# Kernel tuning notes

Hardware: AMD Instinct MI355X
Metric: run time of the kernel (lower is better)

Reference implementation:

```python
import jax, jax.numpy as jnp
import numpy as np

B, T, C, H = 2, 2048, 1024, 16
HD = C // H            # 64
LAYER_IDX, N_LAYER = 5, 12
BASE = 16
# window_mode='power_2.0': progress=(5+1)/12=0.5; window=max(16, int(16+0.5**2*(2048-16)))=524
WINDOW = max(BASE, int(BASE + ((LAYER_IDX + 1) / N_LAYER) ** 2.0 * (T - BASE)))
WINDOW = min(WINDOW, T)


def setup_inputs() -> dict:
    key = jax.random.key(0)
    ks = jax.random.split(key, 6)
    x = jax.random.normal(ks[0], (B, T, C), dtype=jnp.float32)
    Wq = jax.random.normal(ks[1], (C, C), dtype=jnp.float32) * 0.02
    Wk = jax.random.normal(ks[2], (C, C), dtype=jnp.float32) * 0.02
    Wv = jax.random.normal(ks[3], (C, C), dtype=jnp.float32) * 0.02
    Wo = jax.random.normal(ks[4], (C, C), dtype=jnp.float32) * 0.02
    # RoPE tables: angles theta_i = t / 10000^(i/(HD/2)), shape (T,1,HD//2) to broadcast over (B,T,H,HD//2)
    half = HD // 2
    inv_freq = 1.0 / (10000.0 ** (jnp.arange(half, dtype=jnp.float32) / half))
    ang = jnp.arange(T, dtype=jnp.float32)[:, None] * inv_freq[None, :]  # (T, half)
    rope_cos = jnp.cos(ang)[:, None, :]  # (T,1,half)
    rope_sin = jnp.sin(ang)[:, None, :]
    return {"x": x, "Wq": Wq, "Wk": Wk, "Wv": Wv, "Wo": Wo,
            "rope_cos": rope_cos, "rope_sin": rope_sin}


def _apply_rotary(x, cos, sin):
    d = x.shape[-1] // 2
    x1, x2 = x[..., :d], x[..., d:]
    return jnp.concatenate([x1 * cos + x2 * sin, -x2 * sin + x1 * cos], axis=-1)


def reference(x, Wq, Wk, Wv, Wo, rope_cos, rope_sin):
    Bv, Tv, Cv = x.shape
    q = (x @ Wq).reshape(Bv, Tv, H, HD)
    k = (x @ Wk).reshape(Bv, Tv, H, HD)
    v = (x @ Wv).reshape(Bv, Tv, H, HD)
    q = _apply_rotary(q, rope_cos, rope_sin)
    k = _apply_rotary(k, rope_cos, rope_sin)
    # sliding-window causal mask: cols<=rows and cols>=rows-WINDOW+1
    rows = jnp.arange(Tv)[:, None]
    cols = jnp.arange(Tv)[None, :]
    allowed = (cols <= rows) & (cols >= rows - WINDOW + 1)  # (T,T)
    scale = 1.0 / np.sqrt(HD)
    scores = jnp.einsum('bthd,bshd->bhts', q, k) * scale  # (B,H,T,T)
    scores = jnp.where(allowed[None, None], scores, -jnp.inf)
    attn = jax.nn.softmax(scores, axis=-1)
    y = jnp.einsum('bhts,bshd->bthd', attn, v).reshape(Bv, Tv, Cv)
    return y @ Wo
```

## Files before the change

kernel.cpp:

```cpp
#include <hip/hip_runtime.h>
#include <math.h>

typedef unsigned short u16;
typedef unsigned int u32;
typedef __bf16 bf16x8 __attribute__((ext_vector_type(8)));
typedef float f32x4 __attribute__((ext_vector_type(4)));
typedef unsigned short ushort4v __attribute__((ext_vector_type(4)));

#define T_SEQ 2048
#define WIN_M1 523
#define QSCALE 0.180336879f
#define MASKV -1e30f
#define MINIT -3000.0f

__device__ __forceinline__ u16 f2b(float f) {
  union { float f; unsigned int u; } v; v.f = f;
  unsigned int u = v.u;
  u += 0x7FFFu + ((u >> 16) & 1u);
  return (u16)(u >> 16);
}

__device__ __forceinline__ u32 cvtpk(float lo, float hi) {
  u32 r;
  asm("v_cvt_pk_bf16_f32 %0, %1, %2" : "=v"(r) : "v"(lo), "v"(hi));
  return r;
}

__device__ __forceinline__ void load_lds16(const u16* g, u16* l) {
  __builtin_amdgcn_global_load_lds(
      (const __attribute__((address_space(1))) void*)g,
      (__attribute__((address_space(3))) void*)l, 16, 0, 0);
}

__global__ void convert_x_k(const float* __restrict__ x, u16* __restrict__ xb) {
  int i = blockIdx.x * blockDim.x + threadIdx.x;
  float4 v = ((const float4*)x)[i];
  u16* d = xb + i * 4;
  d[0] = f2b(v.x); d[1] = f2b(v.y); d[2] = f2b(v.z); d[3] = f2b(v.w);
}

__global__ void transpose_w4_k(const float* __restrict__ W0, const float* __restrict__ W1,
                               const float* __restrict__ W2, const float* __restrict__ W3,
                               u16* __restrict__ WcatT, u16* __restrict__ WoT) {
  __shared__ float tile[32][33];
  const int z = blockIdx.z;
  const float* W = (z == 0) ? W0 : (z == 1) ? W1 : (z == 2) ? W2 : W3;
  u16* Wt = (z < 3) ? (WcatT + (size_t)z * 1024 * 1024) : WoT;
  int tx = threadIdx.x & 31, ty = threadIdx.x >> 5;
  int n0 = blockIdx.x * 32, k0 = blockIdx.y * 32;
#pragma unroll
  for (int i = 0; i < 4; ++i)
    tile[ty + i * 8][tx] = W[(size_t)(k0 + ty + i * 8) * 1024 + n0 + tx];
  __syncthreads();
#pragma unroll
  for (int i = 0; i < 4; ++i)
    Wt[(size_t)(n0 + ty + i * 8) * 1024 + k0 + tx] = f2b(tile[tx][ty + i * 8]);
}

template <int MODE>
__global__ __launch_bounds__(256, 4) void gemm_k(
    const u16* __restrict__ A, const u16* __restrict__ Bt,
    float* __restrict__ outf,
    u16* __restrict__ Qo, u16* __restrict__ Ko, u16* __restrict__ Vto,
    const float* __restrict__ rc, const float* __restrict__ rs) {
  __shared__ alignas(16) u16 As[2][128 * 32];
  __shared__ alignas(16) u16 Bs[2][128 * 32];
  const int tid = threadIdx.x, lane = tid & 63, w = tid >> 6;
  const int l15 = lane & 15, q4 = lane >> 4;
  const int row0 = blockIdx.y * 128, col0 = blockIdx.x * 128;
  const int wm = w >> 1, wn = w & 1;
  constexpr int NT = 32;

  f32x4 acc[4][4];
#pragma unroll
  for (int i = 0; i < 4; ++i)
#pragma unroll
    for (int j = 0; j < 4; ++j) acc[i][j] = (f32x4){0.f, 0.f, 0.f, 0.f};

  const int off0 = (w * 2) * 1024 + lane * 16;
  const int r0 = off0 >> 6, c0 = (off0 & 63) >> 1;
  const int off1 = off0 + 1024;
  const int r1 = off1 >> 6, c1 = (off1 & 63) >> 1;
  const u16* gA0 = A + (size_t)(row0 + r0) * 1024 + c0;
  const u16* gA1 = A + (size_t)(row0 + r1) * 1024 + c1;
  const u16* gB0 = Bt + (size_t)(col0 + r0) * 1024 + c0;
  const u16* gB1 = Bt + (size_t)(col0 + r1) * 1024 + c1;
  const int soff = (w * 2) * 512;

  auto stage = [&](int buf, int t) {
    const int k0 = t * 32;
    load_lds16(gA0 + k0, &As[buf][soff]);
    load_lds16(gA1 + k0, &As[buf][soff + 512]);
    load_lds16(gB0 + k0, &Bs[buf][soff]);
    load_lds16(gB1 + k0, &Bs[buf][soff + 512]);
  };
  auto compute = [&](int buf) {
    bf16x8 af[4], bfr[4];
#pragma unroll
    for (int im = 0; im < 4; ++im)
      af[im] = *(const bf16x8*)&As[buf][(wm * 64 + im * 16 + l15) * 32 + q4 * 8];
#pragma unroll
    for (int jn = 0; jn < 4; ++jn)
      bfr[jn] = *(const bf16x8*)&Bs[buf][(wn * 64 + jn * 16 + l15) * 32 + q4 * 8];
#pragma unroll
    for (int im = 0; im < 4; ++im)
#pragma unroll
      for (int jn = 0; jn < 4; ++jn)
        acc[im][jn] = __builtin_amdgcn_mfma_f32_16x16x32_bf16(af[im], bfr[jn], acc[im][jn], 0, 0, 0);
  };

  stage(0, 0);
  for (int t = 0; t + 1 < NT; ++t) {
    stage((t + 1) & 1, t + 1);
    asm volatile("s_waitcnt vmcnt(4)" ::: "memory");
    __builtin_amdgcn_s_barrier();
    compute(t & 1);
    __builtin_amdgcn_s_barrier();
  }
  asm volatile("s_waitcnt vmcnt(0)" ::: "memory");
  __builtin_amdgcn_s_barrier();
  compute((NT - 1) & 1);

  if constexpr (MODE == 0) {
#pragma unroll
    for (int im = 0; im < 4; ++im) {
      const int rowb = row0 + wm * 64 + im * 16 + q4 * 4;
      const int b = rowb >> 11, t0 = rowb & 2047;
#pragma unroll
      for (int jn = 0; jn < 2; ++jn) {
        const int n = col0 + wn * 64 + jn * 16 + l15;
        const int sel = n >> 10, nn = n & 1023;
        const int h = nn >> 6, hd = nn & 63;
        if (sel < 2) {
          const float qs = (sel == 0) ? QSCALE : 1.0f;
          u16* dst = (sel == 0 ? Qo : Ko) + ((size_t)(b * 16 + h) * 2048) * 64;
#pragma unroll
          for (int r = 0; r < 4; ++r) {
            const int tt = t0 + r;
            const float c = rc[tt * 32 + hd], s = rs[tt * 32 + hd];
            const float x1 = acc[im][jn][r], x2 = acc[im][jn + 2][r];
            dst[(size_t)tt * 64 + hd] = f2b((x1 * c + x2 * s) * qs);
            dst[(size_t)tt * 64 + hd + 32] = f2b((x1 * c - x2 * s) * qs);
          }
        } else {
          ushort4v p1, p2;
#pragma unroll
          for (int r = 0; r < 4; ++r) {
            p1[r] = f2b(acc[im][jn][r]);
            p2[r] = f2b(acc[im][jn + 2][r]);
          }
          u16* dst = Vto + (size_t)(b * 16 + h) * 64 * 2048 + t0;
          *(ushort4v*)(dst + (size_t)hd * 2048) = p1;
          *(ushort4v*)(dst + (size_t)(hd + 32) * 2048) = p2;
        }
      }
    }
  } else {
#pragma unroll
    for (int im = 0; im < 4; ++im) {
      const int rowb = row0 + wm * 64 + im * 16 + q4 * 4;
#pragma unroll
      for (int jn = 0; jn < 4; ++jn) {
        const int n = col0 + wn * 64 + jn * 16 + l15;
#pragma unroll
        for (int r = 0; r < 4; ++r)
          outf[(size_t)(rowb + r) * 1024 + n] = acc[im][jn][r];
      }
    }
  }
}

__global__ __launch_bounds__(256) void attn_k(
    const u16* __restrict__ Q, const u16* __restrict__ Kk,
    const u16* __restrict__ Vt, u16* __restrict__ Y) {
  const int lane = threadIdx.x & 63, w = threadIdx.x >> 6;
  const int l15 = lane & 15, q4 = lane >> 4;
  const int qt = blockIdx.x & 15, bh = blockIdx.x >> 4;
  const int q0 = qt * 128 + w * 32;
  const u16* Qb = Q + (size_t)bh * 2048 * 64;
  const u16* Kb = Kk + (size_t)bh * 2048 * 64;
  const u16* Vb = Vt + (size_t)bh * 64 * 2048;

  bf16x8 bq[2][2];
#pragma unroll
  for (int qs = 0; qs < 2; ++qs)
#pragma unroll
    for (int kb = 0; kb < 2; ++kb)
      bq[qs][kb] = *(const bf16x8*)(Qb + (size_t)(q0 + qs * 16 + l15) * 64 + kb * 32 + q4 * 8);

  f32x4 o[2][4];
#pragma unroll
  for (int qs = 0; qs < 2; ++qs)
#pragma unroll
    for (int jo = 0; jo < 4; ++jo) o[qs][jo] = (f32x4){0.f, 0.f, 0.f, 0.f};
  float m[2] = {MINIT, MINIT}, lsum[2] = {0.f, 0.f};

  int s0 = q0 - WIN_M1; if (s0 < 0) s0 = 0; s0 &= ~31;
  const int srcA = l15 + ((q4 & 1) << 5);
  const int srcB = srcA + 16;
  const bool lowq4 = (q4 < 2);

  bf16x8 kc[2][2], kn[2][2];
  bf16x8 vc[4], vn[4];
#pragma unroll
  for (int ks = 0; ks < 2; ++ks)
#pragma unroll
    for (int kb = 0; kb < 2; ++kb)
      kc[ks][kb] = *(const bf16x8*)(Kb + (size_t)(s0 + ks * 16 + l15) * 64 + kb * 32 + q4 * 8);
#pragma unroll
  for (int jo = 0; jo < 4; ++jo)
    vc[jo] = *(const bf16x8*)(Vb + (size_t)(jo * 16 + l15) * 2048 + s0 + q4 * 8);

  int kv0 = s0;

#define TILE_BODY(KC, VC, KN, VN)                                                      \
  {                                                                                    \
    const int kvn = kv0 + 32;                                                          \
    if (kvn <= q0) {                                                                   \
      _Pragma("unroll") for (int ks = 0; ks < 2; ++ks)                                 \
          _Pragma("unroll") for (int kb = 0; kb < 2; ++kb)                             \
              KN[ks][kb] = *(const bf16x8*)(Kb + (size_t)(kvn + ks * 16 + l15) * 64 +  \
                                            kb * 32 + q4 * 8);                         \
      _Pragma("unroll") for (int jo = 0; jo < 4; ++jo)                                 \
          VN[jo] = *(const bf16x8*)(Vb + (size_t)(jo * 16 + l15) * 2048 + kvn +        \
                                    q4 * 8);                                           \
    }                                                                                  \
    f32x4 ss[2][2];                                                                    \
    _Pragma("unroll") for (int ks = 0; ks < 2; ++ks)                                   \
        _Pragma("unroll") for (int qs = 0; qs < 2; ++qs)                               \
            ss[ks][qs] = (f32x4){0.f, 0.f, 0.f, 0.f};                                  \
    _Pragma("unroll") for (int kb = 0; kb < 2; ++kb)                                   \
        _Pragma("unroll") for (int ks = 0; ks < 2; ++ks)                               \
            _Pragma("unroll") for (int qs = 0; qs < 2; ++qs)                           \
                ss[ks][qs] = __builtin_amdgcn_mfma_f32_16x16x32_bf16(                  \
                    KC[ks][kb], bq[qs][kb], ss[ks][qs], 0, 0, 0);                      \
    if ((kv0 + 32 > q0) || (kv0 < q0 - 492)) {                                         \
      _Pragma("unroll") for (int qs = 0; qs < 2; ++qs) {                               \
        const int tq = q0 + qs * 16 + l15;                                             \
        _Pragma("unroll") for (int ks = 0; ks < 2; ++ks)                               \
            _Pragma("unroll") for (int r = 0; r < 4; ++r) {                            \
          const int kv = kv0 + ks * 16 + q4 * 4 + r;                                   \
          if (kv > tq || kv < tq - WIN_M1) ss[ks][qs][r] = MASKV;                      \
        }                                                                              \
      }                                                                                \
    }                                                                                  \
    float tmax[2];                                                                     \
    _Pragma("unroll") for (int qs = 0; qs < 2; ++qs) {                                 \
      float a = fmaxf(fmaxf(ss[0][qs][0], ss[0][qs][1]),                               \
                      fmaxf(ss[0][qs][2], ss[0][qs][3]));                              \
      float b = fmaxf(fmaxf(ss[1][qs][0], ss[1][qs][1]),                               \
                      fmaxf(ss[1][qs][2], ss[1][qs][3]));                              \
      float tm = fmaxf(a, b);                                                          \
      tm = fmaxf(tm, __shfl_xor(tm, 16));                                              \
      tm = fmaxf(tm, __shfl_xor(tm, 32));                                              \
      tmax[qs] = tm;                                                                   \
    }                                                                                  \
    const int pred = (tmax[0] <= m[0] + 8.f) && (tmax[1] <= m[1] + 8.f);               \
    if (!__all(pred)) {                                                                \
      _Pragma("unroll") for (int qs = 0; qs < 2; ++qs) {                               \
        const float mn = fmaxf(m[qs], tmax[qs]);                                       \
        const float sc = exp2f(m[qs] - mn);                                            \
        m[qs] = mn; lsum[qs] *= sc;                                                    \
        _Pragma("unroll") for (int r = 0; r < 4; ++r) {                                \
          const float sr = __shfl(sc, q4 * 4 + r);                                     \
          _Pragma("unroll") for (int jo = 0; jo < 4; ++jo) o[qs][jo][r] *= sr;         \
        }                                                                              \
      }                                                                                \
    }                                                                                  \
    _Pragma("unroll") for (int qs = 0; qs < 2; ++qs) {                                 \
      const float mm = m[qs];                                                          \
      float p[2][4];                                                                   \
      _Pragma("unroll") for (int ks = 0; ks < 2; ++ks)                                 \
          _Pragma("unroll") for (int r = 0; r < 4; ++r)                                \
              p[ks][r] = exp2f(ss[ks][qs][r] - mm);                                    \
      float rsv = ((p[0][0] + p[0][1]) + (p[0][2] + p[0][3])) +                        \
                  ((p[1][0] + p[1][1]) + (p[1][2] + p[1][3]));                         \
      rsv += __shfl_xor(rsv, 16);                                                      \
      rsv += __shfl_xor(rsv, 32);                                                      \
      lsum[qs] += rsv;                                                                 \
      const u32 a0 = cvtpk(p[0][0], p[0][1]), a1 = cvtpk(p[0][2], p[0][3]);            \
      const u32 b0 = cvtpk(p[1][0], p[1][1]), b1 = cvtpk(p[1][2], p[1][3]);            \
      union { u32 d[4]; bf16x8 v; } pu;                                                \
      const u32 d0a = (u32)__shfl((int)a0, srcA), d0b = (u32)__shfl((int)b0, srcA);    \
      const u32 d1a = (u32)__shfl((int)a1, srcA), d1b = (u32)__shfl((int)b1, srcA);    \
      const u32 d2a = (u32)__shfl((int)a0, srcB), d2b = (u32)__shfl((int)b0, srcB);    \
      const u32 d3a = (u32)__shfl((int)a1, srcB), d3b = (u32)__shfl((int)b1, srcB);    \
      pu.d[0] = lowq4 ? d0a : d0b;                                                     \
      pu.d[1] = lowq4 ? d1a : d1b;                                                     \
      pu.d[2] = lowq4 ? d2a : d2b;                                                     \
      pu.d[3] = lowq4 ? d3a : d3b;                                                     \
      _Pragma("unroll") for (int jo = 0; jo < 4; ++jo)                                 \
          o[qs][jo] = __builtin_amdgcn_mfma_f32_16x16x32_bf16(pu.v, VC[jo],            \
                                                              o[qs][jo], 0, 0, 0);     \
    }                                                                                  \
  }

  while (true) {
    TILE_BODY(kc, vc, kn, vn);
    kv0 += 32; if (kv0 > q0) break;
    TILE_BODY(kn, vn, kc, vc);
    kv0 += 32; if (kv0 > q0) break;
  }
#undef TILE_BODY

  const int b = bh >> 4, h = bh & 15;
  u16* Yb = Y + (size_t)(b * 2048 + q0) * 1024 + h * 64 + l15;
#pragma unroll
  for (int qs = 0; qs < 2; ++qs)
#pragma unroll
    for (int r = 0; r < 4; ++r) {
      const float lv = __shfl(lsum[qs], q4 * 4 + r);
      const float inv = 1.0f / lv;
      u16* yr = Yb + (size_t)(qs * 16 + q4 * 4 + r) * 1024;
#pragma unroll
      for (int jo = 0; jo < 4; ++jo) yr[jo * 16] = f2b(o[qs][jo][r] * inv);
    }
}

extern "C" void kernel_launch(void* const* d_in, const int* in_sizes, int n_in,
                              void* d_out, int out_size, void* d_ws, size_t ws_size,
                              hipStream_t stream) {
  const float* x = (const float*)d_in[0];
  const float* Wq = (const float*)d_in[1];
  const float* Wk = (const float*)d_in[2];
  const float* Wv = (const float*)d_in[3];
  const float* Wo = (const float*)d_in[4];
  const float* rc = (const float*)d_in[5];
  const float* rs = (const float*)d_in[6];
  float* out = (float*)d_out;
  char* ws = (char*)d_ws;
  const size_t MB = 1024 * 1024;
  u16* xb = (u16*)(ws);
  u16* WcatT = (u16*)(ws + 8 * MB);
  u16* WoT = (u16*)(ws + 14 * MB);
  u16* Qr = (u16*)(ws + 16 * MB);
  u16* Kr = (u16*)(ws + 24 * MB);
  u16* Vt = (u16*)(ws + 32 * MB);
  u16* Y = (u16*)(ws + 40 * MB);

  convert_x_k<<<4096, 256, 0, stream>>>(x, xb);
  transpose_w4_k<<<dim3(32, 32, 4), 256, 0, stream>>>(Wq, Wk, Wv, Wo, WcatT, WoT);
  gemm_k<0><<<dim3(24, 32), 256, 0, stream>>>(xb, WcatT, nullptr, Qr, Kr, Vt, rc, rs);
  attn_k<<<512, 256, 0, stream>>>(Qr, Kr, Vt, Y);
  gemm_k<1><<<dim3(8, 32), 256, 0, stream>>>(Y, WoT, out, nullptr, nullptr, nullptr, nullptr, nullptr);
}
```

Before: 112.4 us.

## Split attention work to 16 query rows per wave and remap blocks

Each wave now handles 16 query rows instead of 32, doubling the attention grid to 1024 blocks, with a block-index swizzle that interleaves work across (batch,head) groups. Launch bounds now request 4 blocks per multiprocessor for better occupancy and load balance across the causal/window triangle. The trade-off is that each K/V tile is loaded and reused for only half as many queries, which increases global/L2 traffic per query.

New measurement: 166.8 us. 48.4% more time.

```diff
diff --git a/kernel.cpp b/kernel.cpp
--- a/kernel.cpp
+++ b/kernel.cpp
@@ -170,32 +170,31 @@
   }
 }
 
-__global__ __launch_bounds__(256) void attn_k(
+__global__ __launch_bounds__(256, 4) void attn_k(
     const u16* __restrict__ Q, const u16* __restrict__ Kk,
     const u16* __restrict__ Vt, u16* __restrict__ Y) {
   const int lane = threadIdx.x & 63, w = threadIdx.x >> 6;
   const int l15 = lane & 15, q4 = lane >> 4;
-  const int qt = blockIdx.x & 15, bh = blockIdx.x >> 4;
-  const int q0 = qt * 128 + w * 32;
+  const int hw = blockIdx.x;
+  const int work = (hw & 7) * 128 + (hw >> 3);
+  const int bh = work >> 5, qt = work & 31;
+  const int q0 = qt * 64 + w * 16;
   const u16* Qb = Q + (size_t)bh * 2048 * 64;
   const u16* Kb = Kk + (size_t)bh * 2048 * 64;
   const u16* Vb = Vt + (size_t)bh * 64 * 2048;
 
-  bf16x8 bq[2][2];
-#pragma unroll
-  for (int qs = 0; qs < 2; ++qs)
-#pragma unroll
-    for (int kb = 0; kb < 2; ++kb)
-      bq[qs][kb] = *(const bf16x8*)(Qb + (size_t)(q0 + qs * 16 + l15) * 64 + kb * 32 + q4 * 8);
-
-  f32x4 o[2][4];
-#pragma unroll
-  for (int qs = 0; qs < 2; ++qs)
-#pragma unroll
-    for (int jo = 0; jo < 4; ++jo) o[qs][jo] = (f32x4){0.f, 0.f, 0.f, 0.f};
-  float m[2] = {MINIT, MINIT}, lsum[2] = {0.f, 0.f};
+  bf16x8 bq[2];
+#pragma unroll
+  for (int kb = 0; kb < 2; ++kb)
+    bq[kb] = *(const bf16x8*)(Qb + (size_t)(q0 + l15) * 64 + kb * 32 + q4 * 8);
+
+  f32x4 o[4];
+#pragma unroll
+  for (int jo = 0; jo < 4; ++jo) o[jo] = (f32x4){0.f, 0.f, 0.f, 0.f};
+  float m = MINIT, lsum = 0.f;
 
   int s0 = q0 - WIN_M1; if (s0 < 0) s0 = 0; s0 &= ~31;
+  const int qend = q0 + 15;
   const int srcA = l15 + ((q4 & 1) << 5);
   const int srcB = srcA + 16;
   const bool lowq4 = (q4 < 2);
@@ -216,7 +215,7 @@
 #define TILE_BODY(KC, VC, KN, VN)                                                      \
   {                                                                                    \
     const int kvn = kv0 + 32;                                                          \
-    if (kvn <= q0) {                                                                   \
+    if (kvn <= qend) {                                                                 \
       _Pragma("unroll") for (int ks = 0; ks < 2; ++ks)                                 \
           _Pragma("unroll") for (int kb = 0; kb < 2; ++kb)                             \
               KN[ks][kb] = *(const bf16x8*)(Kb + (size_t)(kvn + ks * 16 + l15) * 64 +  \
@@ -225,96 +224,76 @@
           VN[jo] = *(const bf16x8*)(Vb + (size_t)(jo * 16 + l15) * 2048 + kvn +        \
                                     q4 * 8);                                           \
     }                                                                                  \
-    f32x4 ss[2][2];                                                                    \
-    _Pragma("unroll") for (int ks = 0; ks < 2; ++ks)                                   \
-        _Pragma("unroll") for (int qs = 0; qs < 2; ++qs)                               \
-            ss[ks][qs] = (f32x4){0.f, 0.f, 0.f, 0.f};                                  \
+    f32x4 ss[2];                                                                       \
+    ss[0] = (f32x4){0.f, 0.f, 0.f, 0.f};                                               \
+    ss[1] = (f32x4){0.f, 0.f, 0.f, 0.f};                                               \
     _Pragma("unroll") for (int kb = 0; kb < 2; ++kb)                                   \
         _Pragma("unroll") for (int ks = 0; ks < 2; ++ks)                               \
-            _Pragma("unroll") for (int qs = 0; qs < 2; ++qs)                           \
-                ss[ks][qs] = __builtin_amdgcn_mfma_f32_16x16x32_bf16(                  \
-                    KC[ks][kb], bq[qs][kb], ss[ks][qs], 0, 0, 0);                      \
-    if ((kv0 + 32 > q0) || (kv0 < q0 - 492)) {                                         \
-      _Pragma("unroll") for (int qs = 0; qs < 2; ++qs) {                               \
-        const int tq = q0 + qs * 16 + l15;                                             \
-        _Pragma("unroll") for (int ks = 0; ks < 2; ++ks)                               \
-            _Pragma("unroll") for (int r = 0; r < 4; ++r) {                            \
-          const int kv = kv0 + ks * 16 + q4 * 4 + r;                                   \
-          if (kv > tq || kv < tq - WIN_M1) ss[ks][qs][r] = MASKV;                      \
-        }                                                                              \
+            ss[ks] = __builtin_amdgcn_mfma_f32_16x16x32_bf16(KC[ks][kb], bq[kb],       \
+                                                             ss[ks], 0, 0, 0);         \
+    if ((kv0 + 31 > q0) || (kv0 < q0 + 15 - WIN_M1)) {                                 \
+      const int tq = q0 + l15;                                                         \
+      _Pragma("unroll") for (int ks = 0; ks < 2; ++ks)                                 \
+          _Pragma("unroll") for (int r = 0; r < 4; ++r) {                              \
+        const int kv = kv0 + ks * 16 + q4 * 4 + r;                                     \
+        if (kv > tq || kv < tq - WIN_M1) ss[ks][r] = MASKV;                            \
       }                                                                                \
     }                                                                                  \
-    float tmax[2];                                                                     \
-    _Pragma("unroll") for (int qs = 0; qs < 2; ++qs) {                                 \
-      float a = fmaxf(fmaxf(ss[0][qs][0], ss[0][qs][1]),                               \
-                      fmaxf(ss[0][qs][2], ss[0][qs][3]));                              \
-      float b = fmaxf(fmaxf(ss[1][qs][0], ss[1][qs][1]),                               \
-                      fmaxf(ss[1][qs][2], ss[1][qs][3]));                              \
-      float tm = fmaxf(a, b);                                                          \
-      tm = fmaxf(tm, __shfl_xor(tm, 16));                                              \
-      tm = fmaxf(tm, __shfl_xor(tm, 32));                                              \
-      tmax[qs] = tm;                                                                   \
-    }                                                                                  \
-    const int pred = (tmax[0] <= m[0] + 8.f) && (tmax[1] <= m[1] + 8.f);               \
-    if (!__all(pred)) {                                                                \
-      _Pragma("unroll") for (int qs = 0; qs < 2; ++qs) {                               \
-        const float mn = fmaxf(m[qs], tmax[qs]);                                       \
-        const float sc = exp2f(m[qs] - mn);                                            \
-        m[qs] = mn; lsum[qs] *= sc;                                                    \
-        _Pragma("unroll") for (int r = 0; r < 4; ++r) {                                \
-          const float sr = __shfl(sc, q4 * 4 + r);                                     \
-          _Pragma("unroll") for (int jo = 0; jo < 4; ++jo) o[qs][jo][r] *= sr;         \
-        }                                                                              \
+    float tm = fmaxf(fmaxf(fmaxf(ss[0][0], ss[0][1]), fmaxf(ss[0][2], ss[0][3])),      \
+                     fmaxf(fmaxf(ss[1][0], ss[1][1]), fmaxf(ss[1][2], ss[1][3])));     \
+    tm = fmaxf(tm, __shfl_xor(tm, 16));                                                \
+    tm = fmaxf(tm, __shfl_xor(tm, 32));                                                \
+    if (!__all(tm <= m + 8.f)) {                                                       \
+      const float mn = fmaxf(m, tm);                                                   \
+      const float sc = exp2f(m - mn);                                                  \
+      m = mn; lsum *= sc;                                                              \
+      _Pragma("unroll") for (int r = 0; r < 4; ++r) {                                  \
+        const float sr = __shfl(sc, q4 * 4 + r);                                       \
+        _Pragma("unroll") for (int jo = 0; jo < 4; ++jo) o[jo][r] *= sr;               \
       }                                                                                \
     }                                                                                  \
-    _Pragma("unroll") for (int qs = 0; qs < 2; ++qs) {                                 \
-      const float mm = m[qs];                                                          \
-      float p[2][4];                                                                   \
-      _Pragma("unroll") for (int ks = 0; ks < 2; ++ks)                                 \
-          _Pragma("unroll") for (int r = 0; r < 4; ++r)                                \
-              p[ks][r] = exp2f(ss[ks][qs][r] - mm);                                    \
-      float rsv = ((p[0][0] + p[0][1]) + (p[0][2] + p[0][3])) +                        \
-                  ((p[1][0] + p[1][1]) + (p[1][2] + p[1][3]));                         \
-      rsv += __shfl_xor(rsv, 16);                                                      \
-      rsv += __shfl_xor(rsv, 32);                                                      \
-      lsum[qs] += rsv;                                                                 \
-      const u32 a0 = cvtpk(p[0][0], p[0][1]), a1 = cvtpk(p[0][2], p[0][3]);            \
-      const u32 b0 = cvtpk(p[1][0], p[1][1]), b1 = cvtpk(p[1][2], p[1][3]);            \
-      union { u32 d[4]; bf16x8 v; } pu;                                                \
-      const u32 d0a = (u32)__shfl((int)a0, srcA), d0b = (u32)__shfl((int)b0, srcA);    \
-      const u32 d1a = (u32)__shfl((int)a1, srcA), d1b = (u32)__shfl((int)b1, srcA);    \
-      const u32 d2a = (u32)__shfl((int)a0, srcB), d2b = (u32)__shfl((int)b0, srcB);    \
-      const u32 d3a = (u32)__shfl((int)a1, srcB), d3b = (u32)__shfl((int)b1, srcB);    \
-      pu.d[0] = lowq4 ? d0a : d0b;                                                     \
-      pu.d[1] = lowq4 ? d1a : d1b;                                                     \
-      pu.d[2] = lowq4 ? d2a : d2b;                                                     \
-      pu.d[3] = lowq4 ? d3a : d3b;                                                     \
-      _Pragma("unroll") for (int jo = 0; jo < 4; ++jo)                                 \
-          o[qs][jo] = __builtin_amdgcn_mfma_f32_16x16x32_bf16(pu.v, VC[jo],            \
-                                                              o[qs][jo], 0, 0, 0);     \
-    }                                                                                  \
+    float p[2][4];                                                                     \
+    _Pragma("unroll") for (int ks = 0; ks < 2; ++ks)                                   \
+        _Pragma("unroll") for (int r = 0; r < 4; ++r)                                  \
+            p[ks][r] = exp2f(ss[ks][r] - m);                                           \
+    float rsv = ((p[0][0] + p[0][1]) + (p[0][2] + p[0][3])) +                          \
+                ((p[1][0] + p[1][1]) + (p[1][2] + p[1][3]));                           \
+    rsv += __shfl_xor(rsv, 16);                                                        \
+    rsv += __shfl_xor(rsv, 32);                                                        \
+    lsum += rsv;                                                                       \
+    const u32 a0 = cvtpk(p[0][0], p[0][1]), a1 = cvtpk(p[0][2], p[0][3]);              \
+    const u32 b0 = cvtpk(p[1][0], p[1][1]), b1 = cvtpk(p[1][2], p[1][3]);              \
+    union { u32 d[4]; bf16x8 v; } pu;                                                  \
+    const u32 d0a = (u32)__shfl((int)a0, srcA), d0b = (u32)__shfl((int)b0, srcA);      \
+    const u32 d1a = (u32)__shfl((int)a1, srcA), d1b = (u32)__shfl((int)b1, srcA);      \
+    const u32 d2a = (u32)__shfl((int)a0, srcB), d2b = (u32)__shfl((int)b0, srcB);      \
+    const u32 d3a = (u32)__shfl((int)a1, srcB), d3b = (u32)__shfl((int)b1, srcB);      \
+    pu.d[0] = lowq4 ? d0a : d0b;                                                       \
+    pu.d[1] = lowq4 ? d1a : d1b;                                                       \
+    pu.d[2] = lowq4 ? d2a : d2b;                                                       \
+    pu.d[3] = lowq4 ? d3a : d3b;                                                       \
+    _Pragma("unroll") for (int jo = 0; jo < 4; ++jo)                                   \
+        o[jo] = __builtin_amdgcn_mfma_f32_16x16x32_bf16(pu.v, VC[jo], o[jo], 0, 0, 0); \
   }
 
   while (true) {
     TILE_BODY(kc, vc, kn, vn);
-    kv0 += 32; if (kv0 > q0) break;
+    kv0 += 32; if (kv0 > qend) break;
     TILE_BODY(kn, vn, kc, vc);
-    kv0 += 32; if (kv0 > q0) break;
+    kv0 += 32; if (kv0 > qend) break;
   }
 #undef TILE_BODY
 
   const int b = bh >> 4, h = bh & 15;
   u16* Yb = Y + (size_t)(b * 2048 + q0) * 1024 + h * 64 + l15;
 #pragma unroll
-  for (int qs = 0; qs < 2; ++qs)
-#pragma unroll
-    for (int r = 0; r < 4; ++r) {
-      const float lv = __shfl(lsum[qs], q4 * 4 + r);
-      const float inv = 1.0f / lv;
-      u16* yr = Yb + (size_t)(qs * 16 + q4 * 4 + r) * 1024;
-#pragma unroll
-      for (int jo = 0; jo < 4; ++jo) yr[jo * 16] = f2b(o[qs][jo][r] * inv);
-    }
+  for (int r = 0; r < 4; ++r) {
+    const float lv = __shfl(lsum, q4 * 4 + r);
+    const float inv = 1.0f / lv;
+    u16* yr = Yb + (size_t)(q4 * 4 + r) * 1024;
+#pragma unroll
+    for (int jo = 0; jo < 4; ++jo) yr[jo * 16] = f2b(o[jo][r] * inv);
+  }
 }
 
 extern "C" void kernel_launch(void* const* d_in, const int* in_sizes, int n_in,
@@ -341,6 +320,6 @@
   convert_x_k<<<4096, 256, 0, stream>>>(x, xb);
   transpose_w4_k<<<dim3(32, 32, 4), 256, 0, stream>>>(Wq, Wk, Wv, Wo, WcatT, WoT);
   gemm_k<0><<<dim3(24, 32), 256, 0, stream>>>(xb, WcatT, nullptr, Qr, Kr, Vt, rc, rs);
-  attn_k<<<512, 256, 0, stream>>>(Qr, Kr, Vt, Y);
+  attn_k<<<1024, 256, 0, stream>>>(Qr, Kr, Vt, Y);
   gemm_k<1><<<dim3(8, 32), 256, 0, stream>>>(Y, WoT, out, nullptr, nullptr, nullptr, nullptr, nullptr);
 }
```

## Use 16x16x16 MFMA for PV to drop P shuffles, defer row-sum reduction

Applied to the files above, without the earlier changes.

The PV product now uses v_mfma_f32_16x16x16_bf16 through inline asm. The softmax probabilities then already sit in the operand layout, so the eight cross-lane shuffles and selects per tile are gone. V is loaded as bf16x4 halves to match. The per-tile row-sum shuffle reduction becomes a per-lane partial sum that is reduced once at the end, and block indices are remapped (hw&7)*64+(hw>>3) to spread work across XCDs. The cost is inline asm with manual s_nop hazard padding, twice as many smaller MFMAs, and smaller V loads.

Result: slower. 126.4 us (+12.4%).

```diff
diff --git a/kernel.cpp b/kernel.cpp
--- a/kernel.cpp
+++ b/kernel.cpp
@@ -4,6 +4,7 @@
 typedef unsigned short u16;
 typedef unsigned int u32;
 typedef __bf16 bf16x8 __attribute__((ext_vector_type(8)));
+typedef __bf16 bf16x4 __attribute__((ext_vector_type(4)));
 typedef float f32x4 __attribute__((ext_vector_type(4)));
 typedef unsigned short ushort4v __attribute__((ext_vector_type(4)));
 
@@ -175,7 +176,9 @@
     const u16* __restrict__ Vt, u16* __restrict__ Y) {
   const int lane = threadIdx.x & 63, w = threadIdx.x >> 6;
   const int l15 = lane & 15, q4 = lane >> 4;
-  const int qt = blockIdx.x & 15, bh = blockIdx.x >> 4;
+  const int hw = blockIdx.x;
+  const int work = (hw & 7) * 64 + (hw >> 3);
+  const int bh = work >> 4, qt = work & 15;
   const int q0 = qt * 128 + w * 32;
   const u16* Qb = Q + (size_t)bh * 2048 * 64;
   const u16* Kb = Kk + (size_t)bh * 2048 * 64;
@@ -193,15 +196,13 @@
   for (int qs = 0; qs < 2; ++qs)
 #pragma unroll
     for (int jo = 0; jo < 4; ++jo) o[qs][jo] = (f32x4){0.f, 0.f, 0.f, 0.f};
-  float m[2] = {MINIT, MINIT}, lsum[2] = {0.f, 0.f};
+  float m[2] = {MINIT, MINIT};
+  float lp[2] = {0.f, 0.f};
 
   int s0 = q0 - WIN_M1; if (s0 < 0) s0 = 0; s0 &= ~31;
-  const int srcA = l15 + ((q4 & 1) << 5);
-  const int srcB = srcA + 16;
-  const bool lowq4 = (q4 < 2);
 
   bf16x8 kc[2][2], kn[2][2];
-  bf16x8 vc[4], vn[4];
+  bf16x4 vc[4][2], vn[4][2];
 #pragma unroll
   for (int ks = 0; ks < 2; ++ks)
 #pragma unroll
@@ -209,7 +210,9 @@
       kc[ks][kb] = *(const bf16x8*)(Kb + (size_t)(s0 + ks * 16 + l15) * 64 + kb * 32 + q4 * 8);
 #pragma unroll
   for (int jo = 0; jo < 4; ++jo)
-    vc[jo] = *(const bf16x8*)(Vb + (size_t)(jo * 16 + l15) * 2048 + s0 + q4 * 8);
+#pragma unroll
+    for (int ks = 0; ks < 2; ++ks)
+      vc[jo][ks] = *(const bf16x4*)(Vb + (size_t)(jo * 16 + l15) * 2048 + s0 + ks * 16 + q4 * 4);
 
   int kv0 = s0;
 
@@ -222,8 +225,9 @@
               KN[ks][kb] = *(const bf16x8*)(Kb + (size_t)(kvn + ks * 16 + l15) * 64 +  \
                                             kb * 32 + q4 * 8);                         \
       _Pragma("unroll") for (int jo = 0; jo < 4; ++jo)                                 \
-          VN[jo] = *(const bf16x8*)(Vb + (size_t)(jo * 16 + l15) * 2048 + kvn +        \
-                                    q4 * 8);                                           \
+          _Pragma("unroll") for (int ks = 0; ks < 2; ++ks)                             \
+              VN[jo][ks] = *(const bf16x4*)(Vb + (size_t)(jo * 16 + l15) * 2048 +      \
+                                            kvn + ks * 16 + q4 * 4);                   \
     }                                                                                  \
     f32x4 ss[2][2];                                                                    \
     _Pragma("unroll") for (int ks = 0; ks < 2; ++ks)                                   \
@@ -260,39 +264,57 @@
       _Pragma("unroll") for (int qs = 0; qs < 2; ++qs) {                               \
         const float mn = fmaxf(m[qs], tmax[qs]);                                       \
         const float sc = exp2f(m[qs] - mn);                                            \
-        m[qs] = mn; lsum[qs] *= sc;                                                    \
+        m[qs] = mn; lp[qs] *= sc;                                                      \
         _Pragma("unroll") for (int r = 0; r < 4; ++r) {                                \
           const float sr = __shfl(sc, q4 * 4 + r);                                     \
           _Pragma("unroll") for (int jo = 0; jo < 4; ++jo) o[qs][jo][r] *= sr;         \
         }                                                                              \
       }                                                                                \
     }                                                                                  \
+    bf16x4 pa[2][2];                                                                   \
     _Pragma("unroll") for (int qs = 0; qs < 2; ++qs) {                                 \
       const float mm = m[qs];                                                          \
       float p[2][4];                                                                   \
       _Pragma("unroll") for (int ks = 0; ks < 2; ++ks)                                 \
           _Pragma("unroll") for (int r = 0; r < 4; ++r)                                \
               p[ks][r] = exp2f(ss[ks][qs][r] - mm);                                    \
-      float rsv = ((p[0][0] + p[0][1]) + (p[0][2] + p[0][3])) +                        \
-                  ((p[1][0] + p[1][1]) + (p[1][2] + p[1][3]));                         \
-      rsv += __shfl_xor(rsv, 16);                                                      \
-      rsv += __shfl_xor(rsv, 32);                                                      \
-      lsum[qs] += rsv;                                                                 \
-      const u32 a0 = cvtpk(p[0][0], p[0][1]), a1 = cvtpk(p[0][2], p[0][3]);            \
-      const u32 b0 = cvtpk(p[1][0], p[1][1]), b1 = cvtpk(p[1][2], p[1][3]);            \
-      union { u32 d[4]; bf16x8 v; } pu;                                                \
-      const u32 d0a = (u32)__shfl((int)a0, srcA), d0b = (u32)__shfl((int)b0, srcA);    \
-      const u32 d1a = (u32)__shfl((int)a1, srcA), d1b = (u32)__shfl((int)b1, srcA);    \
-      const u32 d2a = (u32)__shfl((int)a0, srcB), d2b = (u32)__shfl((int)b0, srcB);    \
-      const u32 d3a = (u32)__shfl((int)a1, srcB), d3b = (u32)__shfl((int)b1, srcB);    \
-      pu.d[0] = lowq4 ? d0a : d0b;                                                     \
-      pu.d[1] = lowq4 ? d1a : d1b;                                                     \
-      pu.d[2] = lowq4 ? d2a : d2b;                                                     \
-      pu.d[3] = lowq4 ? d3a : d3b;                                                     \
-      _Pragma("unroll") for (int jo = 0; jo < 4; ++jo)                                 \
-          o[qs][jo] = __builtin_amdgcn_mfma_f32_16x16x32_bf16(pu.v, VC[jo],            \
-                                                              o[qs][jo], 0, 0, 0);     \
-    }                                                                                  \
+      lp[qs] += ((p[0][0] + p[0][1]) + (p[0][2] + p[0][3])) +                          \
+                ((p[1][0] + p[1][1]) + (p[1][2] + p[1][3]));                           \
+      _Pragma("unroll") for (int ks = 0; ks < 2; ++ks) {                               \
+        union { u32 d[2]; bf16x4 v; } pk;                                              \
+        pk.d[0] = cvtpk(p[ks][0], p[ks][1]);                                           \
+        pk.d[1] = cvtpk(p[ks][2], p[ks][3]);                                           \
+        pa[qs][ks] = pk.v;                                                             \
+      }                                                                                \
+    }                                                                                  \
+    asm volatile(                                                                      \
+        "s_nop 1\n\t"                                                                  \
+        "v_mfma_f32_16x16x16_bf16 %[x00], %[a0], %[b00], %[x00]\n\t"                   \
+        "v_mfma_f32_16x16x16_bf16 %[x01], %[a0], %[b10], %[x01]\n\t"                   \
+        "v_mfma_f32_16x16x16_bf16 %[x02], %[a0], %[b20], %[x02]\n\t"                   \
+        "v_mfma_f32_16x16x16_bf16 %[x03], %[a0], %[b30], %[x03]\n\t"                   \
+        "v_mfma_f32_16x16x16_bf16 %[x10], %[a2], %[b00], %[x10]\n\t"                   \
+        "v_mfma_f32_16x16x16_bf16 %[x11], %[a2], %[b10], %[x11]\n\t"                   \
+        "v_mfma_f32_16x16x16_bf16 %[x12], %[a2], %[b20], %[x12]\n\t"                   \
+        "v_mfma_f32_16x16x16_bf16 %[x13], %[a2], %[b30], %[x13]\n\t"                   \
+        "v_mfma_f32_16x16x16_bf16 %[x00], %[a1], %[b01], %[x00]\n\t"                   \
+        "v_mfma_f32_16x16x16_bf16 %[x01], %[a1], %[b11], %[x01]\n\t"                   \
+        "v_mfma_f32_16x16x16_bf16 %[x02], %[a1], %[b21], %[x02]\n\t"                   \
+        "v_mfma_f32_16x16x16_bf16 %[x03], %[a1], %[b31], %[x03]\n\t"                   \
+        "v_mfma_f32_16x16x16_bf16 %[x10], %[a3], %[b01], %[x10]\n\t"                   \
+        "v_mfma_f32_16x16x16_bf16 %[x11], %[a3], %[b11], %[x11]\n\t"                   \
+        "v_mfma_f32_16x16x16_bf16 %[x12], %[a3], %[b21], %[x12]\n\t"                   \
+        "v_mfma_f32_16x16x16_bf16 %[x13], %[a3], %[b31], %[x13]\n\t"                   \
+        "s_nop 7\n\t"                                                                  \
+        "s_nop 7"                                                                      \
+        : [x00] "+v"(o[0][0]), [x01] "+v"(o[0][1]), [x02] "+v"(o[0][2]),               \
+          [x03] "+v"(o[0][3]), [x10] "+v"(o[1][0]), [x11] "+v"(o[1][1]),               \
+          [x12] "+v"(o[1][2]), [x13] "+v"(o[1][3])                                     \
+        : [a0] "v"(pa[0][0]), [a1] "v"(pa[0][1]), [a2] "v"(pa[1][0]),                  \
+          [a3] "v"(pa[1][1]),                                                          \
+          [b00] "v"(VC[0][0]), [b01] "v"(VC[0][1]), [b10] "v"(VC[1][0]),               \
+          [b11] "v"(VC[1][1]), [b20] "v"(VC[2][0]), [b21] "v"(VC[2][1]),               \
+          [b30] "v"(VC[3][0]), [b31] "v"(VC[3][1]));                                   \
   }
 
   while (true) {
@@ -306,15 +328,19 @@
   const int b = bh >> 4, h = bh & 15;
   u16* Yb = Y + (size_t)(b * 2048 + q0) * 1024 + h * 64 + l15;
 #pragma unroll
-  for (int qs = 0; qs < 2; ++qs)
+  for (int qs = 0; qs < 2; ++qs) {
+    float l = lp[qs];
+    l += __shfl_xor(l, 16);
+    l += __shfl_xor(l, 32);
 #pragma unroll
     for (int r = 0; r < 4; ++r) {
-      const float lv = __shfl(lsum[qs], q4 * 4 + r);
+      const float lv = __shfl(l, q4 * 4 + r);
       const float inv = 1.0f / lv;
       u16* yr = Yb + (size_t)(qs * 16 + q4 * 4 + r) * 1024;
 #pragma unroll
       for (int jo = 0; jo < 4; ++jo) yr[jo * 16] = f2b(o[qs][jo][r] * inv);
     }
+  }
 }
 
 extern "C" void kernel_launch(void* const* d_in, const int* in_sizes, int n_in,
```
